# Kernel tuning notes

Hardware: AMD Instinct MI355X
Metric: run time of the kernel (lower is better)

## Reference

```python
import jax, jax.numpy as jnp
import numpy as np

NUM_EMOTIONS = 8
EMOTION_DIM = 32
MAX_EMOTIONS = 3
HIDDEN = 768
NUM_HEADS = 8
HEAD_DIM = HIDDEN // NUM_HEADS // 2  # 48
DEPTH = 0
LAMBDA_INIT = 0.8 - 0.6 * float(np.exp(-0.3 * DEPTH))  # 0.2
EPS = 1e-5


def setup_inputs() -> dict:
    key = jax.random.key(0)
    ks = jax.random.split(key, 16)
    B = 16384
    emotion_indices = jax.random.randint(ks[0], (B, MAX_EMOTIONS), 0, NUM_EMOTIONS)
    confidence_values = jax.random.uniform(ks[1], (B, MAX_EMOTIONS), dtype=jnp.float32)
    emb_table = jax.random.normal(ks[2], (NUM_EMOTIONS + 1, EMOTION_DIM), jnp.float32)
    emb_table = emb_table.at[NUM_EMOTIONS].set(0.0)  # padding_idx row
    s1 = 1.0 / np.sqrt(EMOTION_DIM)
    s2 = 1.0 / np.sqrt(HIDDEN)
    W1 = jax.random.normal(ks[3], (EMOTION_DIM, HIDDEN), jnp.float32) * s1
    b1 = jnp.zeros((HIDDEN,), jnp.float32)
    ln_g = jnp.ones((HIDDEN,), jnp.float32)
    ln_b = jnp.zeros((HIDDEN,), jnp.float32)
    Wq = jax.random.normal(ks[4], (HIDDEN, HIDDEN), jnp.float32) * s2
    Wk = jax.random.normal(ks[5], (HIDDEN, HIDDEN), jnp.float32) * s2
    Wv = jax.random.normal(ks[6], (HIDDEN, HIDDEN), jnp.float32) * s2
    Wo = jax.random.normal(ks[7], (HIDDEN, HIDDEN), jnp.float32) * s2
    lq1 = jax.random.normal(ks[8], (HEAD_DIM,), jnp.float32) * 0.1
    lk1 = jax.random.normal(ks[9], (HEAD_DIM,), jnp.float32) * 0.1
    lq2 = jax.random.normal(ks[10], (HEAD_DIM,), jnp.float32) * 0.1
    lk2 = jax.random.normal(ks[11], (HEAD_DIM,), jnp.float32) * 0.1
    subln_w = jnp.ones((2 * HEAD_DIM,), jnp.float32)
    return dict(emotion_indices=emotion_indices, confidence_values=confidence_values,
                emb_table=emb_table, W1=W1, b1=b1, ln_g=ln_g, ln_b=ln_b,
                Wq=Wq, Wk=Wk, Wv=Wv, Wo=Wo,
                lq1=lq1, lk1=lk1, lq2=lq2, lk2=lk2, subln_w=subln_w)


def _rotary_tables(seq_len, dim):
    inv_freq = 1.0 / (10000.0 ** (jnp.arange(0, dim, 2, dtype=jnp.float32) / dim))  # [dim/2]
    t = jnp.arange(seq_len, dtype=jnp.float32)
    ang = jnp.outer(t, inv_freq)  # [S, dim/2]
    return jnp.cos(ang), jnp.sin(ang)


def _apply_rope(x, cos, sin):
    # x: [B, S, H, D]; cos/sin: [S, D/2] (interleaved pairs)
    x1, x2 = x[..., 0::2], x[..., 1::2]
    c = cos[None, :, None, :]
    s = sin[None, :, None, :]
    r1 = x1 * c - x2 * s
    r2 = x1 * s + x2 * c
    return jnp.stack([r1, r2], axis=-1).reshape(x.shape)


def _forward(emotion_indices, confidence_values, emb_table, W1, b1, ln_g, ln_b,
             Wq, Wk, Wv, Wo, lq1, lk1, lq2, lk2, subln_w):
    B, S = emotion_indices.shape  # S == MAX_EMOTIONS
    idx = jnp.where(emotion_indices < 0, NUM_EMOTIONS, emotion_indices)

    # embedding lookup + confidence weighting
    emb = emb_table[idx] * confidence_values[..., None]  # [B,S,32]

    # Linear + LayerNorm + GELU (dropout = identity in eval)
    h = emb @ W1 + b1  # [B,S,768]
    mu = jnp.mean(h, axis=-1, keepdims=True)
    var = jnp.mean(jnp.square(h - mu), axis=-1, keepdims=True)
    h = (h - mu) / jnp.sqrt(var + EPS) * ln_g + ln_b
    h = jax.nn.gelu(h, approximate=False)

    # rotary tables
    cos, sin = _rotary_tables(S, HEAD_DIM)

    # additive attention mask: -inf over padded key columns
    pad = (idx == NUM_EMOTIONS)  # [B,S]
    neg_inf = jnp.asarray(-jnp.inf, h.dtype)
    mask = jnp.where(pad[:, None, None, :], neg_inf, 0.0)  # [B,1,1,S] -> bcast to [B,1,S,S]

    # differential attention
    q = (h @ Wq).reshape(B, S, 2 * NUM_HEADS, HEAD_DIM)
    k = (h @ Wk).reshape(B, S, 2 * NUM_HEADS, HEAD_DIM)
    v = (h @ Wv).reshape(B, S, NUM_HEADS, 2 * HEAD_DIM)
    q = _apply_rope(q, cos, sin)
    k = _apply_rope(k, cos, sin)

    scale = HEAD_DIM ** -0.5
    scores = jnp.einsum('bqhd,bkhd->bhqk', q, k) * scale + mask  # [B,2H,S,S]
    attn = jax.nn.softmax(scores, axis=-1)
    attn = attn.reshape(B, NUM_HEADS, 2, S, S)
    lam = (jnp.exp(jnp.sum(lq1 * lk1)) - jnp.exp(jnp.sum(lq2 * lk2)) + LAMBDA_INIT)
    diff = attn[:, :, 0] - lam * attn[:, :, 1]  # [B,H,S,S]

    out = jnp.einsum('bhqk,bkhd->bqhd', diff, v)  # [B,S,H,2d]
    # sublayer RMSNorm over last dim
    rms = jnp.sqrt(jnp.mean(jnp.square(out), axis=-1, keepdims=True) + EPS)
    out = out / rms * subln_w
    out = out * (1.0 - LAMBDA_INIT)
    out = out.reshape(B, S, HIDDEN) @ Wo  # [B,S,768]

    # masked mean pooling over non-padding positions
    npad = (~pad).astype(out.dtype)[..., None]  # [B,S,1]
    summed = jnp.sum(out * npad, axis=1)
    denom = jnp.maximum(jnp.sum(npad, axis=1), 1.0)
    return summed / denom  # [B,768]


def reference(emotion_indices, confidence_values, emb_table, W1, b1, ln_g, ln_b,
              Wq, Wk, Wv, Wo, lq1, lk1, lq2, lk2, subln_w):
    return _forward(emotion_indices, confidence_values, emb_table, W1, b1, ln_g, ln_b,
                    Wq, Wk, Wv, Wo, lq1, lk1, lq2, lk2, subln_w)
```

## Files before the change

kernel.cpp:

```cpp
#include <hip/hip_runtime.h>
#include <hip/hip_bf16.h>
#include <math.h>
#include <stdint.h>

typedef __hip_bfloat16 bf16;
typedef __attribute__((ext_vector_type(8))) short short8;
typedef __attribute__((ext_vector_type(4))) float f32x4;
typedef __attribute__((ext_vector_type(2))) unsigned int u32x2;

#define NB 16384
#define HID 768
#define EPS_LN 1e-5f
#define LAM_INIT 0.2f

__device__ __forceinline__ float bf2f(bf16 x){ return __bfloat162float(x); }
__device__ __forceinline__ bf16  f2bf(float x){ return __float2bfloat16(x); }
__device__ __forceinline__ float bfbits(uint32_t lo16){ return __uint_as_float(lo16 << 16); }
__device__ __forceinline__ uint32_t f2bfbits(float x){
  union { float f; uint32_t u; } v; v.f = x;
  uint32_t u = v.u;
  uint32_t r = (u + 0x7fff + ((u >> 16) & 1)) >> 16;
  return r;
}

template<typename T> __device__ __forceinline__ float ldv(const void* p, int i);
template<> __device__ __forceinline__ float ldv<float>(const void* p, int i){ return ((const float*)p)[i]; }
template<> __device__ __forceinline__ float ldv<bf16 >(const void* p, int i){ return bf2f(((const bf16*)p)[i]); }

template<typename T> __device__ __forceinline__ void stv(T* p, float v);
template<> __device__ __forceinline__ void stv<float>(float* p, float v){ *p = v; }
template<> __device__ __forceinline__ void stv<bf16 >(bf16*  p, float v){ *p = f2bf(v); }

__device__ __forceinline__ void async_copy16(void* lds, const void* g){
  __builtin_amdgcn_global_load_lds(
      (const __attribute__((address_space(1))) unsigned int*)g,
      (__attribute__((address_space(3))) unsigned int*)lds, 16, 0, 0);
}

__device__ __forceinline__ float wred64(float v){
  #pragma unroll
  for (int m = 1; m <= 32; m <<= 1) v += __shfl_xor(v, m, 64);
  return v;
}

__global__ void prep_flag(const void* etab, const void* lq1, const void* lk1,
                          const void* lq2, const void* lk2, float* prep){
  const int lane = threadIdx.x;
  const uint32_t* p = (const uint32_t*)((const char*)etab + 512);
  int v = (lane < 16) ? (int)p[lane] : 0;
  #pragma unroll
  for (int m = 1; m <= 32; m <<= 1) v |= __shfl_xor(v, m, 64);
  const int isbf = (v == 0) ? 1 : 0;
  if (lane == 0) ((int*)prep)[0] = isbf;

  float p1 = 0.f, p2 = 0.f;
  if (lane < 48){
    if (isbf){ p1 = ldv<bf16>(lq1,lane)*ldv<bf16>(lk1,lane); p2 = ldv<bf16>(lq2,lane)*ldv<bf16>(lk2,lane); }
    else     { p1 = ldv<float>(lq1,lane)*ldv<float>(lk1,lane); p2 = ldv<float>(lq2,lane)*ldv<float>(lk2,lane); }
  }
  p1 = wred64(p1); p2 = wred64(p2);
  if (lane == 0) prep[1] = expf(p1) - expf(p2) + LAM_INIT;

  if (lane < 24){
    float invf = powf(10000.f, -(float)(2*lane)/48.f);
    #pragma unroll
    for (int s=0;s<3;++s){
      float ang = (float)s*invf;
      float c = cosf(ang), sv = sinf(ang);
      prep[16  + s*32 + lane] = c;
      prep[128 + s*32 + lane] = sv;
      prep[256 + (s*24 + lane)*2    ] = c;
      prep[256 + (s*24 + lane)*2 + 1] = sv;
    }
  }
}

template<typename T>
__device__ __forceinline__ void prep_e1_body(const void* etab, const void* W1,
                                             const void* b1, float* prep,
                                             float (*red)[4]){
  const int id  = blockIdx.x;
  const int tid = threadIdx.x;
  const int wave = tid >> 6, lane = tid & 63;

  float et[32];
  #pragma unroll
  for (int e=0;e<32;++e) et[e] = ldv<T>(etab, id*32+e);

  float su=0.f, suu=0.f, sub=0.f;
  #pragma unroll
  for (int q=0;q<3;++q){
    const int cc = tid + q*256;
    float s = 0.f;
    #pragma unroll
    for (int e=0;e<32;++e) s += et[e]*ldv<T>(W1, e*HID+cc);
    prep[1024 + id*HID + cc] = s;
    float bv = ldv<T>(b1, cc);
    su += s; suu += s*s; sub += s*bv;
  }
  su = wred64(su); suu = wred64(suu); sub = wred64(sub);
  if (lane==0){ red[0][wave]=su; red[1][wave]=suu; red[2][wave]=sub; }
  __syncthreads();
  if (tid==0){
    float a=0.f,b=0.f,c=0.f;
    #pragma unroll
    for (int w=0;w<4;++w){ a+=red[0][w]; b+=red[1][w]; c+=red[2][w]; }
    prep[512+id]=a*(1.f/768.f); prep[528+id]=b*(1.f/768.f); prep[544+id]=c*(1.f/768.f);
  }
  if (id==0){
    float sb=0.f, sbb=0.f;
    #pragma unroll
    for (int q=0;q<3;++q){ float bv=ldv<T>(b1, tid+q*256); sb+=bv; sbb+=bv*bv; }
    sb=wred64(sb); sbb=wred64(sbb);
    __syncthreads();
    if (lane==0){ red[0][wave]=sb; red[1][wave]=sbb; }
    __syncthreads();
    if (tid==0){
      float a=0.f,b=0.f;
      #pragma unroll
      for (int w=0;w<4;++w){ a+=red[0][w]; b+=red[1][w]; }
      prep[560]=a*(1.f/768.f); prep[561]=b*(1.f/768.f);
    }
  }
}

__global__ __launch_bounds__(256) void prep_e1(const void* etab, const void* W1,
                                               const void* b1, float* prep){
  __shared__ float red[3][4];
  if (((const int*)prep)[0]) prep_e1_body<bf16 >(etab, W1, b1, prep, red);
  else                       prep_e1_body<float>(etab, W1, b1, prep, red);
}

template<typename T>
__device__ __forceinline__ void transpose_body(bf16 (*tile)[33], const void* src, bf16* dst){
  const int n0 = blockIdx.x*32, k0 = blockIdx.y*32;
  const int tx = threadIdx.x, ty = threadIdx.y;
  #pragma unroll
  for (int r=0;r<4;++r)
    tile[ty + 8*r][tx] = f2bf(ldv<T>(src, (k0 + ty + 8*r)*HID + n0 + tx));
  __syncthreads();
  #pragma unroll
  for (int r=0;r<4;++r)
    dst[(size_t)(n0 + ty + 8*r)*HID + k0 + tx] = tile[tx][ty + 8*r];
}

__global__ __launch_bounds__(256) void transpose_weights(
    const void* Wq, const void* Wk, const void* Wv, const void* Wo,
    bf16* __restrict__ WqkvT, bf16* __restrict__ WoT, const float* prep)
{
  __shared__ bf16 tile[32][33];
  const int z = blockIdx.z;
  const void* src = (z==0)? Wq : (z==1)? Wk : (z==2)? Wv : Wo;
  bf16* dst = (z<3)? (WqkvT + (size_t)z*HID*HID) : WoT;
  if (((const int*)prep)[0]) transpose_body<bf16 >(tile, src, dst);
  else                       transpose_body<float>(tile, src, dst);
}

template<typename T>
__device__ __forceinline__ void embed_body(
    const int* eidx, const void* conf, const void* b1, const void* lng,
    const void* lnb, const float* prep, bf16* hout, int tok0)
{
  const int wave = threadIdx.x >> 6, lane = threadIdx.x & 63;
  const int t0 = blockIdx.x*16 + wave*4;
  const int c  = lane*12;
  float bb[12], gg[12], be[12];
  #pragma unroll
  for (int d=0;d<12;++d){ bb[d]=ldv<T>(b1,c+d); gg[d]=ldv<T>(lng,c+d); be[d]=ldv<T>(lnb,c+d); }
  const float m_b = prep[560], s_bb = prep[561];
  const float* E1 = prep + 1024;

  #pragma unroll
  for (int tt = 0; tt < 4; ++tt){
    const int tl = t0 + tt, tg = tok0 + tl;
    int id = eidx[tg]; if (id < 0) id = 8;
    const float cf = ldv<T>(conf, tg);
    const float4* ep = (const float4*)(E1 + id*HID + c);
    float4 u0 = ep[0], u1 = ep[1], u2 = ep[2];
    float u[12] = {u0.x,u0.y,u0.z,u0.w, u1.x,u1.y,u1.z,u1.w, u2.x,u2.y,u2.z,u2.w};
    const float mu  = cf*prep[512+id] + m_b;
    const float ex2 = cf*cf*prep[528+id] + 2.f*cf*prep[544+id] + s_bb;
    const float var = ex2 - mu*mu;
    const float rs  = rsqrtf(fmaxf(var, 0.f) + EPS_LN);
    uint32_t w[6];
    #pragma unroll
    for (int d=0;d<6;++d){
      float x0 = cf*u[2*d]   + bb[2*d];
      float x1 = cf*u[2*d+1] + bb[2*d+1];
      float y0 = (x0-mu)*rs*gg[2*d]   + be[2*d];
      float y1 = (x1-mu)*rs*gg[2*d+1] + be[2*d+1];
      float g0 = 0.5f*y0*(1.f + erff(y0*0.70710678118f));
      float g1 = 0.5f*y1*(1.f + erff(y1*0.70710678118f));
      w[d] = f2bfbits(g0) | (f2bfbits(g1) << 16);
    }
    char* op = (char*)hout + (size_t)(tl*HID + c)*2;
    ((u32x2*)op)[0] = (u32x2){w[0],w[1]};
    ((u32x2*)op)[1] = (u32x2){w[2],w[3]};
    ((u32x2*)op)[2] = (u32x2){w[4],w[5]};
  }
}

__global__ __launch_bounds__(256) void embed_ln_gelu(
    const int* __restrict__ eidx, const void* conf, const void* b1,
    const void* lng, const void* lnb, const float* prep,
    bf16* __restrict__ hout, int tok0)
{
  if (((const int*)prep)[0]) embed_body<bf16 >(eidx, conf, b1, lng, lnb, prep, hout, tok0);
  else                       embed_body<float>(eidx, conf, b1, lng, lnb, prep, hout, tok0);
}

template<typename OutT>
__device__ __forceinline__ void gemm_body(
    bf16* sA, bf16* sB,
    const bf16* __restrict__ A, const bf16* __restrict__ Bt, OutT* __restrict__ C,
    int K, int lda, int ldb, int ldc, int MT, int NT)
{
  int bid = blockIdx.x;
  int mt, nt;
  if ((MT & 7) == 0) {
    int x = bid & 7, j = bid >> 3;
    nt = j % NT;
    mt = x * (MT >> 3) + j / NT;
  } else { nt = bid % NT; mt = bid / NT; }

  const int tid = threadIdx.x;
  const int wave = tid >> 6, lane = tid & 63;
  const int m0 = mt * 128, n0 = nt * 128;
  const int wm = wave >> 1, wn = wave & 1;

  f32x4 acc[4][4];
  #pragma unroll
  for (int i=0;i<4;++i)
    #pragma unroll
    for (int j=0;j<4;++j) acc[i][j] = (f32x4){0.f,0.f,0.f,0.f};

  const char* Ag = (const char*)(A  + (size_t)m0 * lda);
  const char* Bg = (const char*)(Bt + (size_t)n0 * ldb);
  const int r8  = lane >> 3;
  const int cBx = ((lane & 7) ^ r8) * 16;

  #define STAGE(buf, kt) do {                                                   \
    _Pragma("unroll")                                                           \
    for (int ii = 0; ii < 4; ++ii) {                                            \
      const int i_ = wave*4 + ii;                                               \
      const int row_ = i_*8 + r8;                                               \
      async_copy16((char*)sA + (buf)*16384 + i_*1024 + lane*16,                 \
                   Ag + ((size_t)row_*lda + (kt))*2 + cBx);                     \
      async_copy16((char*)sB + (buf)*16384 + i_*1024 + lane*16,                 \
                   Bg + ((size_t)row_*ldb + (kt))*2 + cBx);                     \
    }                                                                           \
  } while(0)

  STAGE(0, 0);
  int cur = 0;
  const int rxor = (lane & 7) << 3;
  for (int kt = 0; kt < K; kt += 64) {
    __syncthreads();
    if (kt + 64 < K) STAGE(cur^1, kt + 64);
    const bf16* pA = sA + cur*8192;
    const bf16* pB = sB + cur*8192;
    #pragma unroll
    for (int ks = 0; ks < 64; ks += 32) {
      const int kq = (ks + (lane >> 4)*8) ^ rxor;
      short8 af[4], bfv[4];
      #pragma unroll
      for (int i=0;i<4;++i)
        af[i]  = *(const short8*)&pA[(wm*64 + i*16 + (lane&15))*64 + kq];
      #pragma unroll
      for (int j=0;j<4;++j)
        bfv[j] = *(const short8*)&pB[(wn*64 + j*16 + (lane&15))*64 + kq];
      #pragma unroll
      for (int i=0;i<4;++i)
        #pragma unroll
        for (int j=0;j<4;++j)
          acc[i][j] = __builtin_amdgcn_mfma_f32_16x16x32_bf16(af[i], bfv[j], acc[i][j], 0,0,0);
    }
    cur ^= 1;
  }
  #undef STAGE

  const int rb = (lane>>4)*4, cb = lane & 15;
  #pragma unroll
  for (int i=0;i<4;++i)
    #pragma unroll
    for (int r=0;r<4;++r) {
      const int grow = m0 + wm*64 + i*16 + rb + r;
      OutT* Cp = C + (size_t)grow*ldc + n0 + wn*64 + cb;
      #pragma unroll
      for (int j=0;j<4;++j) stv<OutT>(Cp + j*16, acc[i][j][r]);
    }
}

__global__ __launch_bounds__(256) void gemm_int(
    const bf16* __restrict__ A, const bf16* __restrict__ Bt, bf16* __restrict__ C,
    int K, int lda, int ldb, int ldc, int MT, int NT)
{
  __shared__ __align__(16) bf16 sA[2*128*64];
  __shared__ __align__(16) bf16 sB[2*128*64];
  gemm_body<bf16>(sA, sB, A, Bt, C, K, lda, ldb, ldc, MT, NT);
}

__global__ __launch_bounds__(256) void gemm_final(
    const bf16* __restrict__ A, const bf16* __restrict__ Bt, void* C,
    int K, int lda, int ldb, int ldc, int MT, int NT, const float* prep)
{
  __shared__ __align__(16) bf16 sA[2*128*64];
  __shared__ __align__(16) bf16 sB[2*128*64];
  if (((const int*)prep)[0]) gemm_body<bf16 >(sA, sB, A, Bt, (bf16*)C,  K, lda, ldb, ldc, MT, NT);
  else                       gemm_body<float>(sA, sB, A, Bt, (float*)C, K, lda, ldb, ldc, MT, NT);
}

template<typename T>
__device__ __forceinline__ void attn_body(
    const bf16* __restrict__ qkv, const int* __restrict__ eidx,
    const void* subw, bf16* __restrict__ obar, int b0, const float* prep)
{
  const int bl = blockIdx.x*4 + (threadIdx.x>>6);
  const int bg = b0 + bl;
  const int lane = threadIdx.x & 63;
  const int h  = lane >> 3;
  const int u  = lane & 7;
  const int g  = u >> 2;
  const int qd = u & 3;

  float npad[3];
  #pragma unroll
  for (int s=0;s<3;++s){ int id = eidx[bg*3+s]; npad[s] = (id < 0 || id == 8) ? 0.f : 1.f; }
  float denom = npad[0]+npad[1]+npad[2]; if (denom < 1.f) denom = 1.f;
  const float lam = prep[1];
  const float2* pk = (const float2*)(prep + 256);

  const char* base = (const char*)(qkv + (size_t)bl*3*2304);
  const int qoff = (2*h+g)*48 + qd*12;

  u32x2 qw[3][3], kw[3][3];
  #pragma unroll
  for (int s=0;s<3;++s){
    const char* qp = base + (size_t)(s*2304 + qoff)*2;
    const char* kp = qp + 768*2;
    #pragma unroll
    for (int t=0;t<3;++t){
      qw[s][t] = *(const u32x2*)(qp + t*8);
      kw[s][t] = *(const u32x2*)(kp + t*8);
    }
  }

  float sc[3][3];
  #pragma unroll
  for (int a=0;a<3;++a){ sc[a][0]=0.f; sc[a][1]=0.f; sc[a][2]=0.f; }
  #pragma unroll
  for (int j=0;j<6;++j){
    float qr1[3], qr2[3], kr1[3], kr2[3];
    #pragma unroll
    for (int s=0;s<3;++s){
      float2 cs = pk[s*24 + qd*6 + j];
      uint32_t qu = qw[s][j>>1][j&1], ku = kw[s][j>>1][j&1];
      float q1 = bfbits(qu & 0xffffu), q2 = bfbits(qu >> 16);
      float k1 = bfbits(ku & 0xffffu), k2 = bfbits(ku >> 16);
      qr1[s] = q1*cs.x - q2*cs.y;  qr2[s] = q1*cs.y + q2*cs.x;
      kr1[s] = k1*cs.x - k2*cs.y;  kr2[s] = k1*cs.y + k2*cs.x;
    }
    #pragma unroll
    for (int a=0;a<3;++a)
      #pragma unroll
      for (int b=0;b<3;++b) sc[a][b] += qr1[a]*kr1[b] + qr2[a]*kr2[b];
  }
  #pragma unroll
  for (int a=0;a<3;++a)
    #pragma unroll
    for (int b=0;b<3;++b){
      float v = sc[a][b];
      v += __shfl_xor(v, 1, 64);
      v += __shfl_xor(v, 2, 64);
      sc[a][b] = v;
    }

  const float scale = 0.14433756729740643f;
  float att[3][3];
  #pragma unroll
  for (int a=0;a<3;++a){
    float s0 = sc[a][0]*scale + (npad[0] > 0.f ? 0.f : -1e30f);
    float s1 = sc[a][1]*scale + (npad[1] > 0.f ? 0.f : -1e30f);
    float s2 = sc[a][2]*scale + (npad[2] > 0.f ? 0.f : -1e30f);
    float mx = fmaxf(s0, fmaxf(s1, s2));
    float e0 = expf(s0-mx), e1 = expf(s1-mx), e2 = expf(s2-mx);
    float inv = 1.f/(e0+e1+e2);
    att[a][0]=e0*inv; att[a][1]=e1*inv; att[a][2]=e2*inv;
  }
  float diff[3][3];
  #pragma unroll
  for (int a=0;a<3;++a)
    #pragma unroll
    for (int b=0;b<3;++b){
      float other = __shfl_xor(att[a][b], 4, 64);
      diff[a][b] = (g==0) ? (att[a][b] - lam*other) : (other - lam*att[a][b]);
    }

  const int vd = u*12;
  float vv[3][12];
  #pragma unroll
  for (int s=0;s<3;++s){
    const char* vp = base + (size_t)(s*2304 + 1536 + h*96 + vd)*2;
    #pragma unroll
    for (int t=0;t<3;++t){
      u32x2 w = *(const u32x2*)(vp + t*8);
      vv[s][t*4+0] = bfbits(w[0] & 0xffffu);
      vv[s][t*4+1] = bfbits(w[0] >> 16);
      vv[s][t*4+2] = bfbits(w[1] & 0xffffu);
      vv[s][t*4+3] = bfbits(w[1] >> 16);
    }
  }
  float sw[12];
  #pragma unroll
  for (int d=0;d<12;++d) sw[d] = ldv<T>(subw, vd + d);

  float acc[12];
  #pragma unroll
  for (int d=0;d<12;++d) acc[d] = 0.f;
  #pragma unroll
  for (int a=0;a<3;++a){
    float o[12]; float ss = 0.f;
    #pragma unroll
    for (int d=0;d<12;++d){
      o[d] = diff[a][0]*vv[0][d] + diff[a][1]*vv[1][d] + diff[a][2]*vv[2][d];
      ss += o[d]*o[d];
    }
    ss += __shfl_xor(ss, 1, 64);
    ss += __shfl_xor(ss, 2, 64);
    ss += __shfl_xor(ss, 4, 64);
    float rms = sqrtf(ss*(1.f/96.f) + 1e-5f);
    float kk  = npad[a]*0.8f/rms;
    #pragma unroll
    for (int d=0;d<12;++d) acc[d] += o[d]*kk*sw[d];
  }
  const float idn = 1.f/denom;
  char* op = (char*)obar + (size_t)(bg*HID + h*96 + vd)*2;
  #pragma unroll
  for (int t=0;t<3;++t){
    u32x2 w;
    w[0] = f2bfbits(acc[t*4+0]*idn) | (f2bfbits(acc[t*4+1]*idn) << 16);
    w[1] = f2bfbits(acc[t*4+2]*idn) | (f2bfbits(acc[t*4+3]*idn) << 16);
    *(u32x2*)(op + t*8) = w;
  }
}

__global__ __launch_bounds__(256) void attn_kernel(
    const bf16* __restrict__ qkv, const int* __restrict__ eidx,
    const void* subw, bf16* __restrict__ obar, int b0, const float* prep)
{
  if (((const int*)prep)[0]) attn_body<bf16 >(qkv, eidx, subw, obar, b0, prep);
  else                       attn_body<float>(qkv, eidx, subw, obar, b0, prep);
}

extern "C" void kernel_launch(void* const* d_in, const int* in_sizes, int n_in,
                              void* d_out, int out_size, void* d_ws, size_t ws_size,
                              hipStream_t stream)
{
  const int*  eidx = (const int*) d_in[0];
  const void* conf = d_in[1];
  const void* etab = d_in[2];
  const void* W1   = d_in[3];
  const void* b1   = d_in[4];
  const void* lng  = d_in[5];
  const void* lnb  = d_in[6];
  const void* Wq   = d_in[7];
  const void* Wk   = d_in[8];
  const void* Wv   = d_in[9];
  const void* Wo   = d_in[10];
  const void* lq1  = d_in[11];
  const void* lk1  = d_in[12];
  const void* lq2  = d_in[13];
  const void* lk2  = d_in[14];
  const void* subw = d_in[15];

  const size_t PREP_B = 36864ull;
  const size_t OBAR_B = 25165824ull, WQKVT_B = 3538944ull, WOT_B = 1179648ull;
  const size_t FIXED  = PREP_B + OBAR_B + WQKVT_B + WOT_B;

  char*  ws   = (char*)d_ws;
  float* prep = (float*)ws;
  bf16*  obar = (bf16*)(ws + PREP_B);
  bf16* WqkvT = (bf16*)(ws + PREP_B + OBAR_B);
  bf16* WoT   = (bf16*)(ws + PREP_B + OBAR_B + WQKVT_B);

  int CB = NB;
  while (CB > 128 && FIXED + (size_t)CB*18432ull > ws_size) CB >>= 1;

  bf16* hbuf = (bf16*)(ws + FIXED);
  bf16* qkv  = (bf16*)(ws + FIXED + (size_t)CB*4608ull);

  prep_flag<<<1, 64, 0, stream>>>(etab, lq1, lk1, lq2, lk2, prep);
  prep_e1<<<9, 256, 0, stream>>>(etab, W1, b1, prep);
  transpose_weights<<<dim3(24,24,4), dim3(32,8), 0, stream>>>(Wq, Wk, Wv, Wo, WqkvT, WoT, prep);

  const int nchunks = NB / CB;
  const int ctok = 3*CB;
  for (int c = 0; c < nchunks; ++c) {
    const int b0 = c*CB, tok0 = b0*3;
    const int MT = ctok/128, NT = 18;
    embed_ln_gelu<<<ctok/16, 256, 0, stream>>>(eidx, conf, b1, lng, lnb, prep, hbuf, tok0);
    gemm_int<<<MT*NT, 256, 0, stream>>>(hbuf, WqkvT, qkv, HID, HID, HID, 2304, MT, NT);
    attn_kernel<<<CB/4, 256, 0, stream>>>(qkv, eidx, subw, obar, b0, prep);
  }

  gemm_final<<<128*6, 256, 0, stream>>>(obar, WoT, (void*)d_out, HID, HID, HID, HID, 128, 6, prep);
}
```

Measured before the change: 444.0 us.

## Merge setup kernels, fuse next-chunk embed into attention, shrink GEMM K-tile

The three setup kernels (flag detection, E1 projection, weight transpose) become one launch that splits work by block index, and each block detects the dtype itself. The embed/LN/GELU work for the next chunk is folded into the attention launch as extra blocks, removing a launch per chunk and letting the two overlap. The GEMM K-tile drops from 64 to 32 with a new swizzle and a minimum of 5 blocks per CU, halving LDS use to raise occupancy, at the cost of more barriers per K step. When the whole batch fits in one chunk, the embed fusion only moves the embed into its own earlier launch.

```diff
diff --git a/kernel.cpp b/kernel.cpp
--- a/kernel.cpp
+++ b/kernel.cpp
@@ -43,14 +43,19 @@
   return v;
 }
 
-__global__ void prep_flag(const void* etab, const void* lq1, const void* lk1,
-                          const void* lq2, const void* lk2, float* prep){
+__device__ __forceinline__ int detect_bf(const void* etab){
+  const uint32_t* p = (const uint32_t*)((const char*)etab + 512);
+  uint32_t v = 0;
+  #pragma unroll
+  for (int i = 0; i < 16; ++i) v |= p[i];
+  return v == 0u ? 1 : 0;
+}
+
+
+__device__ __forceinline__ void misc_body(int isbf, const void* lq1, const void* lk1,
+                                          const void* lq2, const void* lk2, float* prep){
   const int lane = threadIdx.x;
-  const uint32_t* p = (const uint32_t*)((const char*)etab + 512);
-  int v = (lane < 16) ? (int)p[lane] : 0;
-  #pragma unroll
-  for (int m = 1; m <= 32; m <<= 1) v |= __shfl_xor(v, m, 64);
-  const int isbf = (v == 0) ? 1 : 0;
+  if (lane >= 64) return;
   if (lane == 0) ((int*)prep)[0] = isbf;
 
   float p1 = 0.f, p2 = 0.f;
@@ -76,10 +81,9 @@
 }
 
 template<typename T>
-__device__ __forceinline__ void prep_e1_body(const void* etab, const void* W1,
+__device__ __forceinline__ void prep_e1_body(int id, const void* etab, const void* W1,
                                              const void* b1, float* prep,
                                              float (*red)[4]){
-  const int id  = blockIdx.x;
   const int tid = threadIdx.x;
   const int wave = tid >> 6, lane = tid & 63;
 
@@ -124,17 +128,11 @@
   }
 }
 
-__global__ __launch_bounds__(256) void prep_e1(const void* etab, const void* W1,
-                                               const void* b1, float* prep){
-  __shared__ float red[3][4];
-  if (((const int*)prep)[0]) prep_e1_body<bf16 >(etab, W1, b1, prep, red);
-  else                       prep_e1_body<float>(etab, W1, b1, prep, red);
-}
-
 template<typename T>
-__device__ __forceinline__ void transpose_body(bf16 (*tile)[33], const void* src, bf16* dst){
-  const int n0 = blockIdx.x*32, k0 = blockIdx.y*32;
-  const int tx = threadIdx.x, ty = threadIdx.y;
+__device__ __forceinline__ void transpose_body(bf16 (*tile)[33], const void* src,
+                                               bf16* dst, int n0, int k0){
+  const int tid = threadIdx.x;
+  const int tx = tid & 31, ty = tid >> 5;
   #pragma unroll
   for (int r=0;r<4;++r)
     tile[ty + 8*r][tx] = f2bf(ldv<T>(src, (k0 + ty + 8*r)*HID + n0 + tx));
@@ -144,25 +142,38 @@
     dst[(size_t)(n0 + ty + 8*r)*HID + k0 + tx] = tile[tx][ty + 8*r];
 }
 
-__global__ __launch_bounds__(256) void transpose_weights(
+__global__ __launch_bounds__(256) void setup_kernel(
+    const void* etab, const void* W1, const void* b1,
+    const void* lq1, const void* lk1, const void* lq2, const void* lk2,
     const void* Wq, const void* Wk, const void* Wv, const void* Wo,
-    bf16* __restrict__ WqkvT, bf16* __restrict__ WoT, const float* prep)
+    bf16* __restrict__ WqkvT, bf16* __restrict__ WoT, float* prep)
 {
   __shared__ bf16 tile[32][33];
-  const int z = blockIdx.z;
-  const void* src = (z==0)? Wq : (z==1)? Wk : (z==2)? Wv : Wo;
-  bf16* dst = (z<3)? (WqkvT + (size_t)z*HID*HID) : WoT;
-  if (((const int*)prep)[0]) transpose_body<bf16 >(tile, src, dst);
-  else                       transpose_body<float>(tile, src, dst);
+  __shared__ float red[3][4];
+  const int bid = blockIdx.x;
+  const int isbf = detect_bf(etab);
+  if (bid < 2304){
+    const int z = bid / 576, rem = bid % 576;
+    const int bx = rem % 24, by = rem / 24;
+    const void* src = (z==0)? Wq : (z==1)? Wk : (z==2)? Wv : Wo;
+    bf16* dst = (z<3)? (WqkvT + (size_t)z*HID*HID) : WoT;
+    if (isbf) transpose_body<bf16 >(tile, src, dst, bx*32, by*32);
+    else      transpose_body<float>(tile, src, dst, bx*32, by*32);
+  } else if (bid == 2304){
+    misc_body(isbf, lq1, lk1, lq2, lk2, prep);
+  } else {
+    if (isbf) prep_e1_body<bf16 >(bid-2305, etab, W1, b1, prep, red);
+    else      prep_e1_body<float>(bid-2305, etab, W1, b1, prep, red);
+  }
 }
 
 template<typename T>
 __device__ __forceinline__ void embed_body(
-    const int* eidx, const void* conf, const void* b1, const void* lng,
+    int bid, const int* eidx, const void* conf, const void* b1, const void* lng,
     const void* lnb, const float* prep, bf16* hout, int tok0)
 {
   const int wave = threadIdx.x >> 6, lane = threadIdx.x & 63;
-  const int t0 = blockIdx.x*16 + wave*4;
+  const int t0 = bid*16 + wave*4;
   const int c  = lane*12;
   float bb[12], gg[12], be[12];
   #pragma unroll
@@ -200,122 +211,12 @@
   }
 }
 
-__global__ __launch_bounds__(256) void embed_ln_gelu(
-    const int* __restrict__ eidx, const void* conf, const void* b1,
-    const void* lng, const void* lnb, const float* prep,
-    bf16* __restrict__ hout, int tok0)
-{
-  if (((const int*)prep)[0]) embed_body<bf16 >(eidx, conf, b1, lng, lnb, prep, hout, tok0);
-  else                       embed_body<float>(eidx, conf, b1, lng, lnb, prep, hout, tok0);
-}
-
-template<typename OutT>
-__device__ __forceinline__ void gemm_body(
-    bf16* sA, bf16* sB,
-    const bf16* __restrict__ A, const bf16* __restrict__ Bt, OutT* __restrict__ C,
-    int K, int lda, int ldb, int ldc, int MT, int NT)
-{
-  int bid = blockIdx.x;
-  int mt, nt;
-  if ((MT & 7) == 0) {
-    int x = bid & 7, j = bid >> 3;
-    nt = j % NT;
-    mt = x * (MT >> 3) + j / NT;
-  } else { nt = bid % NT; mt = bid / NT; }
-
-  const int tid = threadIdx.x;
-  const int wave = tid >> 6, lane = tid & 63;
-  const int m0 = mt * 128, n0 = nt * 128;
-  const int wm = wave >> 1, wn = wave & 1;
-
-  f32x4 acc[4][4];
-  #pragma unroll
-  for (int i=0;i<4;++i)
-    #pragma unroll
-    for (int j=0;j<4;++j) acc[i][j] = (f32x4){0.f,0.f,0.f,0.f};
-
-  const char* Ag = (const char*)(A  + (size_t)m0 * lda);
-  const char* Bg = (const char*)(Bt + (size_t)n0 * ldb);
-  const int r8  = lane >> 3;
-  const int cBx = ((lane & 7) ^ r8) * 16;
-
-  #define STAGE(buf, kt) do {                                                   \
-    _Pragma("unroll")                                                           \
-    for (int ii = 0; ii < 4; ++ii) {                                            \
-      const int i_ = wave*4 + ii;                                               \
-      const int row_ = i_*8 + r8;                                               \
-      async_copy16((char*)sA + (buf)*16384 + i_*1024 + lane*16,                 \
-                   Ag + ((size_t)row_*lda + (kt))*2 + cBx);                     \
-      async_copy16((char*)sB + (buf)*16384 + i_*1024 + lane*16,                 \
-                   Bg + ((size_t)row_*ldb + (kt))*2 + cBx);                     \
-    }                                                                           \
-  } while(0)
-
-  STAGE(0, 0);
-  int cur = 0;
-  const int rxor = (lane & 7) << 3;
-  for (int kt = 0; kt < K; kt += 64) {
-    __syncthreads();
-    if (kt + 64 < K) STAGE(cur^1, kt + 64);
-    const bf16* pA = sA + cur*8192;
-    const bf16* pB = sB + cur*8192;
-    #pragma unroll
-    for (int ks = 0; ks < 64; ks += 32) {
-      const int kq = (ks + (lane >> 4)*8) ^ rxor;
-      short8 af[4], bfv[4];
-      #pragma unroll
-      for (int i=0;i<4;++i)
-        af[i]  = *(const short8*)&pA[(wm*64 + i*16 + (lane&15))*64 + kq];
-      #pragma unroll
-      for (int j=0;j<4;++j)
-        bfv[j] = *(const short8*)&pB[(wn*64 + j*16 + (lane&15))*64 + kq];
-      #pragma unroll
-      for (int i=0;i<4;++i)
-        #pragma unroll
-        for (int j=0;j<4;++j)
-          acc[i][j] = __builtin_amdgcn_mfma_f32_16x16x32_bf16(af[i], bfv[j], acc[i][j], 0,0,0);
-    }
-    cur ^= 1;
-  }
-  #undef STAGE
-
-  const int rb = (lane>>4)*4, cb = lane & 15;
-  #pragma unroll
-  for (int i=0;i<4;++i)
-    #pragma unroll
-    for (int r=0;r<4;++r) {
-      const int grow = m0 + wm*64 + i*16 + rb + r;
-      OutT* Cp = C + (size_t)grow*ldc + n0 + wn*64 + cb;
-      #pragma unroll
-      for (int j=0;j<4;++j) stv<OutT>(Cp + j*16, acc[i][j][r]);
-    }
-}
-
-__global__ __launch_bounds__(256) void gemm_int(
-    const bf16* __restrict__ A, const bf16* __restrict__ Bt, bf16* __restrict__ C,
-    int K, int lda, int ldb, int ldc, int MT, int NT)
-{
-  __shared__ __align__(16) bf16 sA[2*128*64];
-  __shared__ __align__(16) bf16 sB[2*128*64];
-  gemm_body<bf16>(sA, sB, A, Bt, C, K, lda, ldb, ldc, MT, NT);
-}
-
-__global__ __launch_bounds__(256) void gemm_final(
-    const bf16* __restrict__ A, const bf16* __restrict__ Bt, void* C,
-    int K, int lda, int ldb, int ldc, int MT, int NT, const float* prep)
-{
-  __shared__ __align__(16) bf16 sA[2*128*64];
-  __shared__ __align__(16) bf16 sB[2*128*64];
-  if (((const int*)prep)[0]) gemm_body<bf16 >(sA, sB, A, Bt, (bf16*)C,  K, lda, ldb, ldc, MT, NT);
-  else                       gemm_body<float>(sA, sB, A, Bt, (float*)C, K, lda, ldb, ldc, MT, NT);
-}
-
 template<typename T>
 __device__ __forceinline__ void attn_body(
-    const bf16* __restrict__ qkv, const int* __restrict__ eidx,
+    int bid, const bf16* __restrict__ qkv, const int* __restrict__ eidx,
     const void* subw, bf16* __restrict__ obar, int b0, const float* prep)
 {
-  const int bl = blockIdx.x*4 + (threadIdx.x>>6);
+  const int bl = bid*4 + (threadIdx.x>>6);
   const int bg = b0 + bl;
   const int lane = threadIdx.x & 63;
   const int h  = lane >> 3;
@@ -444,12 +345,118 @@
   }
 }
 
-__global__ __launch_bounds__(256) void attn_kernel(
-    const bf16* __restrict__ qkv, const int* __restrict__ eidx,
-    const void* subw, bf16* __restrict__ obar, int b0, const float* prep)
-{
-  if (((const int*)prep)[0]) attn_body<bf16 >(qkv, eidx, subw, obar, b0, prep);
-  else                       attn_body<float>(qkv, eidx, subw, obar, b0, prep);
+__global__ __launch_bounds__(256) void attn_embed(
+    const bf16* __restrict__ qkv, const int* __restrict__ eidx, const void* subw,
+    bf16* __restrict__ obar, int b0, const float* prep,
+    const void* conf, const void* b1, const void* lng, const void* lnb,
+    bf16* __restrict__ hout, int tok0e, int nattn)
+{
+  const int isbf = ((const int*)prep)[0];
+  if ((int)blockIdx.x < nattn){
+    if (isbf) attn_body<bf16 >(blockIdx.x, qkv, eidx, subw, obar, b0, prep);
+    else      attn_body<float>(blockIdx.x, qkv, eidx, subw, obar, b0, prep);
+  } else {
+    const int eb = blockIdx.x - nattn;
+    if (isbf) embed_body<bf16 >(eb, eidx, conf, b1, lng, lnb, prep, hout, tok0e);
+    else      embed_body<float>(eb, eidx, conf, b1, lng, lnb, prep, hout, tok0e);
+  }
+}
+
+template<typename OutT>
+__device__ __forceinline__ void gemm_body(
+    bf16* sA, bf16* sB,
+    const bf16* __restrict__ A, const bf16* __restrict__ Bt, OutT* __restrict__ C,
+    int K, int lda, int ldb, int ldc, int MT, int NT)
+{
+  int bid = blockIdx.x;
+  int mt, nt;
+  if ((MT & 7) == 0) {
+    int x = bid & 7, j = bid >> 3;
+    nt = j % NT;
+    mt = x * (MT >> 3) + j / NT;
+  } else { nt = bid % NT; mt = bid / NT; }
+
+  const int tid = threadIdx.x;
+  const int lane = tid & 63;
+  const int wave = tid >> 6;
+  const int m0 = mt * 128, n0 = nt * 128;
+  const int wm = wave >> 1, wn = wave & 1;
+
+  f32x4 acc[4][4];
+  #pragma unroll
+  for (int i=0;i<4;++i)
+    #pragma unroll
+    for (int j=0;j<4;++j) acc[i][j] = (f32x4){0.f,0.f,0.f,0.f};
+
+  const char* Ag = (const char*)(A  + (size_t)m0 * lda);
+  const char* Bg = (const char*)(Bt + (size_t)n0 * ldb);
+  const int srow = tid >> 2;
+  const int csw  = ((tid & 3) ^ ((tid >> 2) & 3)) * 16;
+
+  #define STAGE(buf, kt) do {                                                   \
+    _Pragma("unroll")                                                           \
+    for (int ii = 0; ii < 2; ++ii) {                                            \
+      const int row_ = ii*64 + srow;                                            \
+      async_copy16((char*)sA + (buf)*8192 + ii*4096 + tid*16,                   \
+                   Ag + ((size_t)row_*lda + (kt))*2 + csw);                     \
+      async_copy16((char*)sB + (buf)*8192 + ii*4096 + tid*16,                   \
+                   Bg + ((size_t)row_*ldb + (kt))*2 + csw);                     \
+    }                                                                           \
+  } while(0)
+
+  STAGE(0, 0);
+  int cur = 0;
+  const int rxor8 = (((lane >> 4) ^ (lane & 3))) * 8;
+  for (int kt = 0; kt < K; kt += 32) {
+    __syncthreads();
+    if (kt + 32 < K) STAGE(cur^1, kt + 32);
+    const bf16* pA = sA + cur*4096;
+    const bf16* pB = sB + cur*4096;
+    short8 af[4], bfv[4];
+    #pragma unroll
+    for (int i=0;i<4;++i)
+      af[i]  = *(const short8*)&pA[(wm*64 + i*16 + (lane&15))*32 + rxor8];
+    #pragma unroll
+    for (int j=0;j<4;++j)
+      bfv[j] = *(const short8*)&pB[(wn*64 + j*16 + (lane&15))*32 + rxor8];
+    #pragma unroll
+    for (int i=0;i<4;++i)
+      #pragma unroll
+      for (int j=0;j<4;++j)
+        acc[i][j] = __builtin_amdgcn_mfma_f32_16x16x32_bf16(af[i], bfv[j], acc[i][j], 0,0,0);
+    cur ^= 1;
+  }
+  #undef STAGE
+
+  const int rb = (lane>>4)*4, cb = lane & 15;
+  #pragma unroll
+  for (int i=0;i<4;++i)
+    #pragma unroll
+    for (int r=0;r<4;++r) {
+      const int grow = m0 + wm*64 + i*16 + rb + r;
+      OutT* Cp = C + (size_t)grow*ldc + n0 + wn*64 + cb;
+      #pragma unroll
+      for (int j=0;j<4;++j) stv<OutT>(Cp + j*16, acc[i][j][r]);
+    }
+}
+
+__global__ __launch_bounds__(256, 5) void gemm_int(
+    const bf16* __restrict__ A, const bf16* __restrict__ Bt, bf16* __restrict__ C,
+    int K, int lda, int ldb, int ldc, int MT, int NT)
+{
+  __shared__ __align__(16) bf16 sA[2*128*32];
+  __shared__ __align__(16) bf16 sB[2*128*32];
+  gemm_body<bf16>(sA, sB, A, Bt, C, K, lda, ldb, ldc, MT, NT);
+}
+
+__global__ __launch_bounds__(256, 5) void gemm_final(
+    const bf16* __restrict__ A, const bf16* __restrict__ Bt, void* C,
+    int K, int lda, int ldb, int ldc, int MT, int NT, const float* prep)
+{
+  __shared__ __align__(16) bf16 sA[2*128*32];
+  __shared__ __align__(16) bf16 sB[2*128*32];
+  if (((const int*)prep)[0]) gemm_body<bf16 >(sA, sB, A, Bt, (bf16*)C,  K, lda, ldb, ldc, MT, NT);
+  else                       gemm_body<float>(sA, sB, A, Bt, (float*)C, K, lda, ldb, ldc, MT, NT);
 }
 
 extern "C" void kernel_launch(void* const* d_in, const int* in_sizes, int n_in,
@@ -489,18 +496,20 @@
   bf16* hbuf = (bf16*)(ws + FIXED);
   bf16* qkv  = (bf16*)(ws + FIXED + (size_t)CB*4608ull);
 
-  prep_flag<<<1, 64, 0, stream>>>(etab, lq1, lk1, lq2, lk2, prep);
-  prep_e1<<<9, 256, 0, stream>>>(etab, W1, b1, prep);
-  transpose_weights<<<dim3(24,24,4), dim3(32,8), 0, stream>>>(Wq, Wk, Wv, Wo, WqkvT, WoT, prep);
+  setup_kernel<<<2314, 256, 0, stream>>>(etab, W1, b1, lq1, lk1, lq2, lk2,
+                                         Wq, Wk, Wv, Wo, WqkvT, WoT, prep);
 
   const int nchunks = NB / CB;
   const int ctok = 3*CB;
+  attn_embed<<<ctok/16, 256, 0, stream>>>(qkv, eidx, subw, obar, 0, prep,
+                                          conf, b1, lng, lnb, hbuf, 0, 0);
   for (int c = 0; c < nchunks; ++c) {
-    const int b0 = c*CB, tok0 = b0*3;
     const int MT = ctok/128, NT = 18;
-    embed_ln_gelu<<<ctok/16, 256, 0, stream>>>(eidx, conf, b1, lng, lnb, prep, hbuf, tok0);
     gemm_int<<<MT*NT, 256, 0, stream>>>(hbuf, WqkvT, qkv, HID, HID, HID, 2304, MT, NT);
-    attn_kernel<<<CB/4, 256, 0, stream>>>(qkv, eidx, subw, obar, b0, prep);
+    const int na = CB/4;
+    const int ne = (c+1 < nchunks) ? ctok/16 : 0;
+    attn_embed<<<na+ne, 256, 0, stream>>>(qkv, eidx, subw, obar, c*CB, prep,
+                                          conf, b1, lng, lnb, hbuf, (c+1)*ctok, na);
   }
 
   gemm_final<<<128*6, 256, 0, stream>>>(obar, WoT, (void*)d_out, HID, HID, HID, HID, 128, 6, prep);
```

After: 547.6 us. +23.3%, slower.
